# Performance work log

Hardware: AMD Instinct MI355X
Metric: run time of the kernel (lower is better)

Reference implementation:

```python
import jax, jax.numpy as jnp
import numpy as np

N, E, D, IN_DIM, NUM_CLASSES, G, L = 50000, 800000, 128, 128, 10, 64, 3
BN_EPS = 1e-5


def _bn(h, gamma, beta, mean, var):
    # inference-mode batchnorm with running stats
    return (h - mean) * jax.lax.rsqrt(var + BN_EPS) * gamma + beta


def setup_inputs() -> dict:
    key = jax.random.key(0)
    ks = jax.random.split(key, 24)
    s = 0.02
    x = jax.random.normal(ks[0], (N, IN_DIM), dtype=jnp.float32)
    c_2 = jax.random.randint(ks[1], (E,), 0, N)
    u_2 = jax.random.randint(ks[2], (E,), 0, N)
    batch = jnp.sort(jax.random.randint(ks[3], (N,), 0, G))
    inp = {
        "x": x, "c_2": c_2, "u_2": u_2, "batch": batch,
        "We": jax.random.normal(ks[4], (IN_DIM, D)) * s,
        "be": jnp.zeros((D,), jnp.float32),
        # per-layer GIN MLP: Linear(d,2d) -> BN(2d) -> ReLU -> Linear(2d,d)
        "W1": jax.random.normal(ks[5], (L, D, 2 * D)) * s,
        "b1": jnp.zeros((L, 2 * D), jnp.float32),
        "g1": jnp.ones((L, 2 * D), jnp.float32),
        "bt1": jnp.zeros((L, 2 * D), jnp.float32),
        "m1": jax.random.normal(ks[6], (L, 2 * D)) * 0.1,
        "v1": jax.random.uniform(ks[7], (L, 2 * D), minval=0.5, maxval=1.5),
        "W2": jax.random.normal(ks[8], (L, 2 * D, D)) * s,
        "b2": jnp.zeros((L, D), jnp.float32),
        # post-conv BatchNorm(d)
        "g2": jnp.ones((L, D), jnp.float32),
        "bt2": jnp.zeros((L, D), jnp.float32),
        "m2": jax.random.normal(ks[9], (L, D)) * 0.1,
        "v2": jax.random.uniform(ks[10], (L, D), minval=0.5, maxval=1.5),
        # readout: Linear(d,d) -> ReLU -> (dropout off) -> Linear(d,num_classes)
        "Wr1": jax.random.normal(ks[11], (D, D)) * s,
        "br1": jnp.zeros((D,), jnp.float32),
        "Wr2": jax.random.normal(ks[12], (D, NUM_CLASSES)) * s,
        "br2": jnp.zeros((NUM_CLASSES,), jnp.float32),
    }
    return inp


def reference(x, c_2, u_2, batch, We, be, W1, b1, g1, bt1, m1, v1,
              W2, b2, g2, bt2, m2, v2, Wr1, br1, Wr2, br2):
    h = x @ We + be  # [N, D]
    for l in range(L):
        # GINConv (eps=0): h_i <- MLP(h_i + sum_{j->i} h_j)
        agg = jax.ops.segment_sum(h[c_2], u_2, num_segments=N)  # [N, D]
        z = h + agg
        z = jax.nn.relu(_bn(z @ W1[l] + b1[l], g1[l], bt1[l], m1[l], v1[l]))
        z = z @ W2[l] + b2[l]
        h = jax.nn.relu(_bn(z, g2[l], bt2[l], m2[l], v2[l]))
        # dropout: identity in eval mode
    pooled = jax.ops.segment_sum(h, batch, num_segments=G)  # [G, D]
    out = jax.nn.relu(pooled @ Wr1 + br1) @ Wr2 + br2  # [G, num_classes]
    return out
```

## Files before the change

kernel.cpp:

```cpp
#include <hip/hip_runtime.h>

#define BN_EPS 1e-5f

typedef __attribute__((ext_vector_type(8))) short bf16x8;
typedef __attribute__((ext_vector_type(4))) float f32x4;
typedef unsigned int uint32;

__device__ __forceinline__ unsigned short f2bf(float f) {
    unsigned u = __float_as_uint(f);
    u += 0x7FFFu + ((u >> 16) & 1u);
    return (unsigned short)(u >> 16);
}
__device__ __forceinline__ float bf2f(unsigned short u) {
    return __uint_as_float((unsigned)u << 16);
}
__device__ __forceinline__ float lo_bf(uint32 u) { return __uint_as_float(u << 16); }
__device__ __forceinline__ float hi_bf(uint32 u) { return __uint_as_float(u & 0xFFFF0000u); }
__device__ __forceinline__ uint32 pack_bf(float a0, float a1) {
    return ((uint32)f2bf(a1) << 16) | (uint32)f2bf(a0);
}

__global__ __launch_bounds__(256) void count_coarse_kernel(const int* __restrict__ u2,
                                                           int* __restrict__ coarse_cnt, int E) {
    __shared__ int lcnt[256];
    const int tid = threadIdx.x;
    lcnt[tid] = 0;
    __syncthreads();
    const int e0 = blockIdx.x * 4096;
#pragma unroll
    for (int k = 0; k < 16; ++k) {
        int e = e0 + k * 256 + tid;
        if (e < E) atomicAdd(&lcnt[u2[e] >> 8], 1);
    }
    __syncthreads();
    int c = lcnt[tid];
    if (c) atomicAdd(&coarse_cnt[tid], c);
}

__global__ __launch_bounds__(256) void bin_coarse_kernel(const int* __restrict__ u2,
                                                         const int* __restrict__ c2,
                                                         const int* __restrict__ coarse_cnt,
                                                         int* __restrict__ coarse_alloc,
                                                         int* __restrict__ buck, int E, int nc) {
    __shared__ int sbuf[256];
    __shared__ int lcnt[256];
    __shared__ int lbase[256];
    const int tid = threadIdx.x;
    int cv = (tid < nc) ? coarse_cnt[tid] : 0;
    sbuf[tid] = cv;
    __syncthreads();
    for (int off = 1; off < 256; off <<= 1) {
        int x = (tid >= off) ? sbuf[tid - off] : 0;
        __syncthreads();
        sbuf[tid] += x;
        __syncthreads();
    }
    const int cstart = sbuf[tid] - cv;
    lcnt[tid] = 0;
    __syncthreads();
    const int e0 = blockIdx.x * 4096;
    int ue[16];
#pragma unroll
    for (int k = 0; k < 16; ++k) {
        int e = e0 + k * 256 + tid;
        int u = (e < E) ? u2[e] : -1;
        ue[k] = u;
        if (u >= 0) atomicAdd(&lcnt[u >> 8], 1);
    }
    __syncthreads();
    int c0 = lcnt[tid];
    lbase[tid] = cstart + (c0 ? atomicAdd(&coarse_alloc[tid], c0) : 0);
    lcnt[tid] = 0;
    __syncthreads();
#pragma unroll
    for (int k = 0; k < 16; ++k) {
        int e = e0 + k * 256 + tid;
        if (e < E) {
            int u = ue[k];
            int cb = u >> 8;
            int pos = lbase[cb] + atomicAdd(&lcnt[cb], 1);
            buck[pos] = ((u & 255) << 16) | c2[e];
        }
    }
}

__global__ __launch_bounds__(256) void bin_node_kernel(const int* __restrict__ coarse_cnt,
                                                       const int* __restrict__ buck,
                                                       int* __restrict__ node_start,
                                                       int* __restrict__ csr_src, int N, int nc) {
    __shared__ int sbuf[256];
    __shared__ int lcnt[256];
    __shared__ int lcur[256];
    const int cb = blockIdx.x;
    const int tid = threadIdx.x;
    int cv = (tid < nc) ? coarse_cnt[tid] : 0;
    sbuf[tid] = cv;
    __syncthreads();
    for (int off = 1; off < 256; off <<= 1) {
        int x = (tid >= off) ? sbuf[tid - off] : 0;
        __syncthreads();
        sbuf[tid] += x;
        __syncthreads();
    }
    lcnt[tid] = 0;
    __syncthreads();
    const int s = (cb == 0) ? 0 : sbuf[cb - 1];
    const int t_end = sbuf[cb];
    for (int e = s + tid; e < t_end; e += 256)
        atomicAdd(&lcnt[buck[e] >> 16], 1);
    __syncthreads();
    int v = lcnt[tid];
    lcur[tid] = v;
    __syncthreads();
    for (int off = 1; off < 256; off <<= 1) {
        int x = (tid >= off) ? lcur[tid - off] : 0;
        __syncthreads();
        lcur[tid] += x;
        __syncthreads();
    }
    int excl = lcur[tid] - v;
    int gstart = s + excl;
    int idx = cb * 256 + tid;
    if (idx <= N) node_start[idx] = gstart;
    lcur[tid] = gstart;
    __syncthreads();
    for (int e = s + tid; e < t_end; e += 256) {
        int w = buck[e];
        int pos = atomicAdd(&lcur[w >> 16], 1);
        csr_src[pos] = w & 0xFFFF;
    }
}

__global__ __launch_bounds__(256) void aggregate_kernel(const unsigned short* __restrict__ h,
                                                        const int* __restrict__ row_start,
                                                        const int* __restrict__ csr_src,
                                                        unsigned short* __restrict__ h2, int N) {
    int node = blockIdx.x * 4 + (threadIdx.x >> 6);
    int lane = threadIdx.x & 63;
    if (node >= N) return;
    const int q = lane >> 4, sl = lane & 15;

    float a0 = 0.f, a1 = 0.f, a2 = 0.f, a3 = 0.f, a4 = 0.f, a5 = 0.f, a6 = 0.f, a7 = 0.f;
    if (q == 0) {
        uint4 v = ((const uint4*)(h + (size_t)node * 128))[sl];
        a0 = lo_bf(v.x); a1 = hi_bf(v.x); a2 = lo_bf(v.y); a3 = hi_bf(v.y);
        a4 = lo_bf(v.z); a5 = hi_bf(v.z); a6 = lo_bf(v.w); a7 = hi_bf(v.w);
    }

    const int rs = row_start[node], re = row_start[node + 1];
    int e = rs;
    for (; e + 16 <= re; e += 16) {
        int s0 = csr_src[e + q];
        int s1 = csr_src[e + 4 + q];
        int s2 = csr_src[e + 8 + q];
        int s3 = csr_src[e + 12 + q];
        uint4 v0 = ((const uint4*)(h + (size_t)s0 * 128))[sl];
        uint4 v1 = ((const uint4*)(h + (size_t)s1 * 128))[sl];
        uint4 v2 = ((const uint4*)(h + (size_t)s2 * 128))[sl];
        uint4 v3 = ((const uint4*)(h + (size_t)s3 * 128))[sl];
        a0 += (lo_bf(v0.x) + lo_bf(v1.x)) + (lo_bf(v2.x) + lo_bf(v3.x));
        a1 += (hi_bf(v0.x) + hi_bf(v1.x)) + (hi_bf(v2.x) + hi_bf(v3.x));
        a2 += (lo_bf(v0.y) + lo_bf(v1.y)) + (lo_bf(v2.y) + lo_bf(v3.y));
        a3 += (hi_bf(v0.y) + hi_bf(v1.y)) + (hi_bf(v2.y) + hi_bf(v3.y));
        a4 += (lo_bf(v0.z) + lo_bf(v1.z)) + (lo_bf(v2.z) + lo_bf(v3.z));
        a5 += (hi_bf(v0.z) + hi_bf(v1.z)) + (hi_bf(v2.z) + hi_bf(v3.z));
        a6 += (lo_bf(v0.w) + lo_bf(v1.w)) + (lo_bf(v2.w) + lo_bf(v3.w));
        a7 += (hi_bf(v0.w) + hi_bf(v1.w)) + (hi_bf(v2.w) + hi_bf(v3.w));
    }
    for (; e + 8 <= re; e += 8) {
        int s0 = csr_src[e + q];
        int s1 = csr_src[e + 4 + q];
        uint4 v = ((const uint4*)(h + (size_t)s0 * 128))[sl];
        uint4 w = ((const uint4*)(h + (size_t)s1 * 128))[sl];
        a0 += lo_bf(v.x) + lo_bf(w.x); a1 += hi_bf(v.x) + hi_bf(w.x);
        a2 += lo_bf(v.y) + lo_bf(w.y); a3 += hi_bf(v.y) + hi_bf(w.y);
        a4 += lo_bf(v.z) + lo_bf(w.z); a5 += hi_bf(v.z) + hi_bf(w.z);
        a6 += lo_bf(v.w) + lo_bf(w.w); a7 += hi_bf(v.w) + hi_bf(w.w);
    }
    for (; e + 4 <= re; e += 4) {
        int s0 = csr_src[e + q];
        uint4 v = ((const uint4*)(h + (size_t)s0 * 128))[sl];
        a0 += lo_bf(v.x); a1 += hi_bf(v.x); a2 += lo_bf(v.y); a3 += hi_bf(v.y);
        a4 += lo_bf(v.z); a5 += hi_bf(v.z); a6 += lo_bf(v.w); a7 += hi_bf(v.w);
    }
    if (q < re - e) {
        int s0 = csr_src[e + q];
        uint4 v = ((const uint4*)(h + (size_t)s0 * 128))[sl];
        a0 += lo_bf(v.x); a1 += hi_bf(v.x); a2 += lo_bf(v.y); a3 += hi_bf(v.y);
        a4 += lo_bf(v.z); a5 += hi_bf(v.z); a6 += lo_bf(v.w); a7 += hi_bf(v.w);
    }

    a0 += __shfl_xor(a0, 16, 64); a0 += __shfl_xor(a0, 32, 64);
    a1 += __shfl_xor(a1, 16, 64); a1 += __shfl_xor(a1, 32, 64);
    a2 += __shfl_xor(a2, 16, 64); a2 += __shfl_xor(a2, 32, 64);
    a3 += __shfl_xor(a3, 16, 64); a3 += __shfl_xor(a3, 32, 64);
    a4 += __shfl_xor(a4, 16, 64); a4 += __shfl_xor(a4, 32, 64);
    a5 += __shfl_xor(a5, 16, 64); a5 += __shfl_xor(a5, 32, 64);
    a6 += __shfl_xor(a6, 16, 64); a6 += __shfl_xor(a6, 32, 64);
    a7 += __shfl_xor(a7, 16, 64); a7 += __shfl_xor(a7, 32, 64);

    if (q == 0) {
        uint4 o;
        o.x = pack_bf(a0, a1); o.y = pack_bf(a2, a3);
        o.z = pack_bf(a4, a5); o.w = pack_bf(a6, a7);
        ((uint4*)(h2 + (size_t)node * 128))[sl] = o;
    }
}

__global__ void prep_kernel(const float* __restrict__ We, const float* __restrict__ W1,
                            const float* __restrict__ W2,
                            unsigned short* __restrict__ Wte,
                            unsigned short* __restrict__ Wt1,
                            unsigned short* __restrict__ Wt2,
                            const float* __restrict__ be,
                            const float* __restrict__ b1, const float* __restrict__ g1,
                            const float* __restrict__ bt1, const float* __restrict__ m1,
                            const float* __restrict__ v1,
                            const float* __restrict__ b2, const float* __restrict__ g2,
                            const float* __restrict__ bt2, const float* __restrict__ m2,
                            const float* __restrict__ v2,
                            float* __restrict__ sce, float* __restrict__ she,
                            float* __restrict__ sc1, float* __restrict__ sh1,
                            float* __restrict__ sc2, float* __restrict__ sh2, int L) {
    int y = blockIdx.y;
    int t = threadIdx.x;
    if (blockIdx.x == 0) {
        if (y == 0) {
            if (t < 128) { sce[t] = 1.f; she[t] = be[t]; }
        } else if (y <= L) {
            int o = (y - 1) * 256 + t;
            float s = g1[o] * rsqrtf(v1[o] + BN_EPS);
            sc1[o] = s;
            sh1[o] = (b1[o] - m1[o]) * s + bt1[o];
        } else {
            if (t < 128) {
                int o = (y - L - 1) * 128 + t;
                float s = g2[o] * rsqrtf(v2[o] + BN_EPS);
                sc2[o] = s;
                sh2[o] = (b2[o] - m2[o]) * s + bt2[o];
            }
        }
    }
    const float* src;
    unsigned short* dst;
    int K;
    if (y == 0)      { src = We; dst = Wte; K = 128; }
    else if (y <= L) { int l = y - 1;     src = W1 + (size_t)l * 128 * 256; dst = Wt1 + (size_t)l * 128 * 256; K = 128; }
    else             { int l = y - L - 1; src = W2 + (size_t)l * 256 * 128; dst = Wt2 + (size_t)l * 256 * 128; K = 256; }
    int idx = blockIdx.x * 256 + t;
    int OUT = 32768 / K;
    if (y == 0) { if (idx >= 128 * 128) return; OUT = 128; }
    int c = idx / K, k = idx % K;
    unsigned byte = ((unsigned)(idx * 2)) ^ (((unsigned)c & 7u) << 4);
    *(unsigned short*)((char*)dst + byte) = f2bf(src[(size_t)k * OUT + c]);
}

template <int K, int OUT, bool RELU, bool A_F32>
__global__ __launch_bounds__(256) void mfma_gemm_kernel(
    const void* __restrict__ Ap, const unsigned short* __restrict__ Wt,
    const float* __restrict__ scale, const float* __restrict__ shift,
    unsigned short* __restrict__ Cout, int nrows)
{
    constexpr int NT = OUT / 16;
    constexpr int KS = K / 32;
    constexpr int CH = OUT * K / 8;
    __shared__ unsigned short WtLds[OUT * K];

    const int tid = threadIdx.x;
    const int wv = tid >> 6, lane = tid & 63;
    {
#pragma unroll
        for (int i = 0; i < CH / 256; ++i) {
            unsigned chunk = (unsigned)(i * 256 + wv * 64);
            const char* gsrc = (const char*)Wt + (size_t)(chunk + lane) * 16u;
            char* ldst = (char*)WtLds + (size_t)chunk * 16u;
            __builtin_amdgcn_global_load_lds(
                (const __attribute__((address_space(1))) void*)gsrc,
                (__attribute__((address_space(3))) void*)ldst,
                16, 0, 0);
        }
    }

    const int l15 = lane & 15, lhi = lane >> 4;
    const int rbase = blockIdx.x * 128 + wv * 32;
    const int r0 = rbase + l15;
    const int r1 = rbase + 16 + l15;
    const int rr0 = min(r0, nrows - 1);
    const int rr1 = min(r1, nrows - 1);

    bf16x8 bfrag[2][KS];
    if constexpr (A_F32) {
        const float* a0 = (const float*)Ap + (size_t)rr0 * K + lhi * 8;
        const float* a1 = (const float*)Ap + (size_t)rr1 * K + lhi * 8;
#pragma unroll
        for (int ks = 0; ks < KS; ++ks) {
            float4 u0 = *(const float4*)(a0 + ks * 32);
            float4 u1 = *(const float4*)(a0 + ks * 32 + 4);
            float4 w0 = *(const float4*)(a1 + ks * 32);
            float4 w1 = *(const float4*)(a1 + ks * 32 + 4);
            bf16x8 f, g;
            f[0] = (short)f2bf(u0.x); f[1] = (short)f2bf(u0.y);
            f[2] = (short)f2bf(u0.z); f[3] = (short)f2bf(u0.w);
            f[4] = (short)f2bf(u1.x); f[5] = (short)f2bf(u1.y);
            f[6] = (short)f2bf(u1.z); f[7] = (short)f2bf(u1.w);
            g[0] = (short)f2bf(w0.x); g[1] = (short)f2bf(w0.y);
            g[2] = (short)f2bf(w0.z); g[3] = (short)f2bf(w0.w);
            g[4] = (short)f2bf(w1.x); g[5] = (short)f2bf(w1.y);
            g[6] = (short)f2bf(w1.z); g[7] = (short)f2bf(w1.w);
            bfrag[0][ks] = f;
            bfrag[1][ks] = g;
        }
    } else {
        const unsigned short* a0 = (const unsigned short*)Ap + (size_t)rr0 * K + lhi * 8;
        const unsigned short* a1 = (const unsigned short*)Ap + (size_t)rr1 * K + lhi * 8;
#pragma unroll
        for (int ks = 0; ks < KS; ++ks) {
            bfrag[0][ks] = *(const bf16x8*)(a0 + ks * 32);
            bfrag[1][ks] = *(const bf16x8*)(a1 + ks * 32);
        }
    }

    __syncthreads();

    f32x4 acc[2][NT];
#pragma unroll
    for (int g = 0; g < 2; ++g)
#pragma unroll
        for (int nt = 0; nt < NT; ++nt) acc[g][nt] = (f32x4){0.f, 0.f, 0.f, 0.f};

#pragma unroll
    for (int ks = 0; ks < KS; ++ks) {
#pragma unroll
        for (int nt = 0; nt < NT; ++nt) {
            int row = nt * 16 + l15;
            unsigned off = ((unsigned)((row * K + ks * 32 + lhi * 8) * 2)) ^ (((unsigned)(l15 & 7u)) << 4);
            bf16x8 wfrag = *(const bf16x8*)((const char*)WtLds + off);
            acc[0][nt] = __builtin_amdgcn_mfma_f32_16x16x32_bf16(wfrag, bfrag[0][ks], acc[0][nt], 0, 0, 0);
            acc[1][nt] = __builtin_amdgcn_mfma_f32_16x16x32_bf16(wfrag, bfrag[1][ks], acc[1][nt], 0, 0, 0);
        }
    }

    const float4* sc4 = (const float4*)scale;
    const float4* sh4 = (const float4*)shift;
#pragma unroll
    for (int g = 0; g < 2; ++g) {
        const int r = (g == 0) ? r0 : r1;
        if (r >= nrows) continue;
#pragma unroll
        for (int nt = 0; nt < NT; ++nt) {
            float4 sc = sc4[nt * 4 + lhi];
            float4 sh = sh4[nt * 4 + lhi];
            float y0 = acc[g][nt][0] * sc.x + sh.x;
            float y1 = acc[g][nt][1] * sc.y + sh.y;
            float y2 = acc[g][nt][2] * sc.z + sh.z;
            float y3 = acc[g][nt][3] * sc.w + sh.w;
            if (RELU) {
                y0 = fmaxf(y0, 0.f); y1 = fmaxf(y1, 0.f);
                y2 = fmaxf(y2, 0.f); y3 = fmaxf(y3, 0.f);
            }
            size_t o = (size_t)r * OUT + nt * 16 + lhi * 4;
            ushort4 p = make_ushort4(f2bf(y0), f2bf(y1), f2bf(y2), f2bf(y3));
            *(ushort4*)(Cout + o) = p;
        }
    }
}

__global__ __launch_bounds__(128) void pool_kernel(const unsigned short* __restrict__ h,
                                                   const int* __restrict__ batch,
                                                   float* __restrict__ pooled, int N, int chunk) {
    int d = threadIdx.x;
    int start = blockIdx.x * chunk;
    if (start >= N) return;
    int end = min(start + chunk, N);
    float acc = 0.f;
    int g = batch[start];
    for (int r = start; r < end; ++r) {
        int bg = batch[r];
        if (bg != g) {
            atomicAdd(&pooled[g * 128 + d], acc);
            acc = 0.f;
            g = bg;
        }
        acc += bf2f(h[(size_t)r * 128 + d]);
    }
    atomicAdd(&pooled[g * 128 + d], acc);
}

__global__ __launch_bounds__(128) void readout_kernel(const float* __restrict__ pooled,
                                                      const float* __restrict__ Wr1,
                                                      const float* __restrict__ br1,
                                                      const float* __restrict__ Wr2,
                                                      const float* __restrict__ br2,
                                                      float* __restrict__ out) {
    __shared__ float prow[128];
    __shared__ float t[128];
    int g = blockIdx.x, j = threadIdx.x;
    prow[j] = pooled[g * 128 + j];
    __syncthreads();
    float acc = 0.f;
    for (int k = 0; k < 128; ++k) acc += prow[k] * Wr1[k * 128 + j];
    t[j] = fmaxf(acc + br1[j], 0.f);
    __syncthreads();
    if (j < 10) {
        float a2 = 0.f;
        for (int k = 0; k < 128; ++k) a2 += t[k] * Wr2[k * 10 + j];
        out[g * 10 + j] = a2 + br2[j];
    }
}

extern "C" void kernel_launch(void* const* d_in, const int* in_sizes, int n_in,
                              void* d_out, int out_size, void* d_ws, size_t ws_size,
                              hipStream_t stream) {
    const float* x   = (const float*)d_in[0];
    const int* c2    = (const int*)d_in[1];
    const int* u2    = (const int*)d_in[2];
    const int* batch = (const int*)d_in[3];
    const float* We  = (const float*)d_in[4];
    const float* be  = (const float*)d_in[5];
    const float* W1  = (const float*)d_in[6];
    const float* b1  = (const float*)d_in[7];
    const float* g1  = (const float*)d_in[8];
    const float* bt1 = (const float*)d_in[9];
    const float* m1  = (const float*)d_in[10];
    const float* v1  = (const float*)d_in[11];
    const float* W2  = (const float*)d_in[12];
    const float* b2  = (const float*)d_in[13];
    const float* g2  = (const float*)d_in[14];
    const float* bt2 = (const float*)d_in[15];
    const float* m2  = (const float*)d_in[16];
    const float* v2  = (const float*)d_in[17];
    const float* Wr1 = (const float*)d_in[18];
    const float* br1 = (const float*)d_in[19];
    const float* Wr2 = (const float*)d_in[20];
    const float* br2 = (const float*)d_in[21];

    const int N = in_sizes[3];
    const int E = in_sizes[1];
    const int L = in_sizes[7] / 256;
    const int G = out_size / 10;

    const int NC = (N + 255) / 256;

    char* ws = (char*)d_ws;
    size_t off = 0;
    auto alloc = [&](size_t bytes) { char* p = ws + off; off += (bytes + 255) & ~(size_t)255; return p; };
    unsigned short* hb   = (unsigned short*)alloc((size_t)N * 128 * 2);
    unsigned short* h2b  = (unsigned short*)alloc((size_t)N * 128 * 2);
    unsigned short* zb   = (unsigned short*)alloc((size_t)N * 256 * 2);
    unsigned short* Wte  = (unsigned short*)alloc(128 * 128 * 2);
    unsigned short* Wt1  = (unsigned short*)alloc((size_t)L * 256 * 128 * 2);
    unsigned short* Wt2  = (unsigned short*)alloc((size_t)L * 128 * 256 * 2);
    float* sce = (float*)alloc(128 * 4);
    float* she = (float*)alloc(128 * 4);
    float* sc1 = (float*)alloc((size_t)L * 256 * 4);
    float* sh1 = (float*)alloc((size_t)L * 256 * 4);
    float* sc2 = (float*)alloc((size_t)L * 128 * 4);
    float* sh2 = (float*)alloc((size_t)L * 128 * 4);
    float* pooled = (float*)alloc((size_t)G * 128 * 4);
    int* coarse_cnt   = (int*)alloc(512 * 4);
    int* coarse_alloc = coarse_cnt + 256;
    int* node_start   = (int*)alloc((size_t)(N + 1) * 4);
    int* buck         = (int*)alloc((size_t)E * 4);
    int* csr_src      = (int*)alloc((size_t)E * 4);

    const int ebins = (E + 4095) / 4096;

    hipMemsetAsync(coarse_cnt, 0, 512 * 4, stream);
    hipMemsetAsync(pooled, 0, (size_t)G * 128 * 4, stream);
    count_coarse_kernel<<<ebins, 256, 0, stream>>>(u2, coarse_cnt, E);
    bin_coarse_kernel<<<ebins, 256, 0, stream>>>(u2, c2, coarse_cnt, coarse_alloc, buck, E, NC);
    bin_node_kernel<<<NC, 256, 0, stream>>>(coarse_cnt, buck, node_start, csr_src, N, NC);

    prep_kernel<<<dim3((256 * 128 + 255) / 256, 1 + 2 * L), 256, 0, stream>>>(
        We, W1, W2, Wte, Wt1, Wt2,
        be, b1, g1, bt1, m1, v1, b2, g2, bt2, m2, v2,
        sce, she, sc1, sh1, sc2, sh2, L);

    const int gemm_blocks = (N + 127) / 128;

    mfma_gemm_kernel<128, 128, false, true><<<gemm_blocks, 256, 0, stream>>>(
        x, Wte, sce, she, hb, N);

    for (int l = 0; l < L; ++l) {
        aggregate_kernel<<<(N + 3) / 4, 256, 0, stream>>>(hb, node_start, csr_src, h2b, N);
        mfma_gemm_kernel<128, 256, true, false><<<gemm_blocks, 256, 0, stream>>>(
            h2b, Wt1 + (size_t)l * 128 * 256, sc1 + l * 256, sh1 + l * 256, zb, N);
        mfma_gemm_kernel<256, 128, true, false><<<gemm_blocks, 256, 0, stream>>>(
            zb, Wt2 + (size_t)l * 256 * 128, sc2 + l * 128, sh2 + l * 128, hb, N);
    }

    const int pool_blocks = 2048;
    const int chunk = (N + pool_blocks - 1) / pool_blocks;
    pool_kernel<<<pool_blocks, 128, 0, stream>>>(hb, batch, pooled, N, chunk);
    readout_kernel<<<G, 128, 0, stream>>>(pooled, Wr1, br1, Wr2, br2, (float*)d_out);
}
```

Before: 277.1 us.

## Split GEMM output columns across waves, shrink row tile to 64

Changes the MFMA GEMM work split: each block now handles 64 rows instead of 128, and each of the four waves computes a quarter of the output columns for all 64 rows instead of all columns for 32 rows. Each LDS weight fragment is reused across four row groups rather than two, and the grid doubles, which helps fill the GPU. The trade-offs are that the full weight matrix is staged into LDS twice as many times in total, each wave loads all 64 A rows (duplicate A reads across waves), and register pressure rises from the larger fragment arrays.

```diff
diff --git a/kernel.cpp b/kernel.cpp
--- a/kernel.cpp
+++ b/kernel.cpp
@@ -261,8 +261,9 @@
     const float* __restrict__ scale, const float* __restrict__ shift,
     unsigned short* __restrict__ Cout, int nrows)
 {
-    constexpr int NT = OUT / 16;
+    constexpr int NT = OUT / 64;
     constexpr int KS = K / 32;
+    constexpr int RG = 4;
     constexpr int CH = OUT * K / 8;
     __shared__ unsigned short WtLds[OUT * K];
 
@@ -282,83 +283,75 @@
     }
 
     const int l15 = lane & 15, lhi = lane >> 4;
-    const int rbase = blockIdx.x * 128 + wv * 32;
-    const int r0 = rbase + l15;
-    const int r1 = rbase + 16 + l15;
-    const int rr0 = min(r0, nrows - 1);
-    const int rr1 = min(r1, nrows - 1);
-
-    bf16x8 bfrag[2][KS];
-    if constexpr (A_F32) {
-        const float* a0 = (const float*)Ap + (size_t)rr0 * K + lhi * 8;
-        const float* a1 = (const float*)Ap + (size_t)rr1 * K + lhi * 8;
-#pragma unroll
-        for (int ks = 0; ks < KS; ++ks) {
-            float4 u0 = *(const float4*)(a0 + ks * 32);
-            float4 u1 = *(const float4*)(a0 + ks * 32 + 4);
-            float4 w0 = *(const float4*)(a1 + ks * 32);
-            float4 w1 = *(const float4*)(a1 + ks * 32 + 4);
-            bf16x8 f, g;
-            f[0] = (short)f2bf(u0.x); f[1] = (short)f2bf(u0.y);
-            f[2] = (short)f2bf(u0.z); f[3] = (short)f2bf(u0.w);
-            f[4] = (short)f2bf(u1.x); f[5] = (short)f2bf(u1.y);
-            f[6] = (short)f2bf(u1.z); f[7] = (short)f2bf(u1.w);
-            g[0] = (short)f2bf(w0.x); g[1] = (short)f2bf(w0.y);
-            g[2] = (short)f2bf(w0.z); g[3] = (short)f2bf(w0.w);
-            g[4] = (short)f2bf(w1.x); g[5] = (short)f2bf(w1.y);
-            g[6] = (short)f2bf(w1.z); g[7] = (short)f2bf(w1.w);
-            bfrag[0][ks] = f;
-            bfrag[1][ks] = g;
-        }
-    } else {
-        const unsigned short* a0 = (const unsigned short*)Ap + (size_t)rr0 * K + lhi * 8;
-        const unsigned short* a1 = (const unsigned short*)Ap + (size_t)rr1 * K + lhi * 8;
-#pragma unroll
-        for (int ks = 0; ks < KS; ++ks) {
-            bfrag[0][ks] = *(const bf16x8*)(a0 + ks * 32);
-            bfrag[1][ks] = *(const bf16x8*)(a1 + ks * 32);
-        }
-    }
-
-    __syncthreads();
-
-    f32x4 acc[2][NT];
-#pragma unroll
-    for (int g = 0; g < 2; ++g)
-#pragma unroll
-        for (int nt = 0; nt < NT; ++nt) acc[g][nt] = (f32x4){0.f, 0.f, 0.f, 0.f};
+    const int wc0 = wv * (OUT / 4);
+    const int rbase = blockIdx.x * 64;
+
+    bf16x8 bfrag[RG][KS];
+#pragma unroll
+    for (int rg = 0; rg < RG; ++rg) {
+        const int rr = min(rbase + rg * 16 + l15, nrows - 1);
+        if constexpr (A_F32) {
+            const float* arow = (const float*)Ap + (size_t)rr * K + lhi * 8;
+#pragma unroll
+            for (int ks = 0; ks < KS; ++ks) {
+                float4 u0 = *(const float4*)(arow + ks * 32);
+                float4 u1 = *(const float4*)(arow + ks * 32 + 4);
+                bf16x8 f;
+                f[0] = (short)f2bf(u0.x); f[1] = (short)f2bf(u0.y);
+                f[2] = (short)f2bf(u0.z); f[3] = (short)f2bf(u0.w);
+                f[4] = (short)f2bf(u1.x); f[5] = (short)f2bf(u1.y);
+                f[6] = (short)f2bf(u1.z); f[7] = (short)f2bf(u1.w);
+                bfrag[rg][ks] = f;
+            }
+        } else {
+            const unsigned short* arow = (const unsigned short*)Ap + (size_t)rr * K + lhi * 8;
+#pragma unroll
+            for (int ks = 0; ks < KS; ++ks)
+                bfrag[rg][ks] = *(const bf16x8*)(arow + ks * 32);
+        }
+    }
+
+    __syncthreads();
+
+    f32x4 acc[RG][NT];
+#pragma unroll
+    for (int rg = 0; rg < RG; ++rg)
+#pragma unroll
+        for (int nt = 0; nt < NT; ++nt) acc[rg][nt] = (f32x4){0.f, 0.f, 0.f, 0.f};
 
 #pragma unroll
     for (int ks = 0; ks < KS; ++ks) {
 #pragma unroll
         for (int nt = 0; nt < NT; ++nt) {
-            int row = nt * 16 + l15;
+            int row = wc0 + nt * 16 + l15;
             unsigned off = ((unsigned)((row * K + ks * 32 + lhi * 8) * 2)) ^ (((unsigned)(l15 & 7u)) << 4);
             bf16x8 wfrag = *(const bf16x8*)((const char*)WtLds + off);
-            acc[0][nt] = __builtin_amdgcn_mfma_f32_16x16x32_bf16(wfrag, bfrag[0][ks], acc[0][nt], 0, 0, 0);
-            acc[1][nt] = __builtin_amdgcn_mfma_f32_16x16x32_bf16(wfrag, bfrag[1][ks], acc[1][nt], 0, 0, 0);
+#pragma unroll
+            for (int rg = 0; rg < RG; ++rg)
+                acc[rg][nt] = __builtin_amdgcn_mfma_f32_16x16x32_bf16(wfrag, bfrag[rg][ks], acc[rg][nt], 0, 0, 0);
         }
     }
 
     const float4* sc4 = (const float4*)scale;
     const float4* sh4 = (const float4*)shift;
 #pragma unroll
-    for (int g = 0; g < 2; ++g) {
-        const int r = (g == 0) ? r0 : r1;
+    for (int rg = 0; rg < RG; ++rg) {
+        const int r = rbase + rg * 16 + l15;
         if (r >= nrows) continue;
 #pragma unroll
         for (int nt = 0; nt < NT; ++nt) {
-            float4 sc = sc4[nt * 4 + lhi];
-            float4 sh = sh4[nt * 4 + lhi];
-            float y0 = acc[g][nt][0] * sc.x + sh.x;
-            float y1 = acc[g][nt][1] * sc.y + sh.y;
-            float y2 = acc[g][nt][2] * sc.z + sh.z;
-            float y3 = acc[g][nt][3] * sc.w + sh.w;
+            const int cq = wc0 / 4 + nt * 4 + lhi;
+            float4 sc = sc4[cq];
+            float4 sh = sh4[cq];
+            float y0 = acc[rg][nt][0] * sc.x + sh.x;
+            float y1 = acc[rg][nt][1] * sc.y + sh.y;
+            float y2 = acc[rg][nt][2] * sc.z + sh.z;
+            float y3 = acc[rg][nt][3] * sc.w + sh.w;
             if (RELU) {
                 y0 = fmaxf(y0, 0.f); y1 = fmaxf(y1, 0.f);
                 y2 = fmaxf(y2, 0.f); y3 = fmaxf(y3, 0.f);
             }
-            size_t o = (size_t)r * OUT + nt * 16 + lhi * 4;
+            size_t o = (size_t)r * OUT + wc0 + nt * 16 + lhi * 4;
             ushort4 p = make_ushort4(f2bf(y0), f2bf(y1), f2bf(y2), f2bf(y3));
             *(ushort4*)(Cout + o) = p;
         }
@@ -476,7 +469,7 @@
         be, b1, g1, bt1, m1, v1, b2, g2, bt2, m2, v2,
         sce, she, sc1, sh1, sc2, sh2, L);
 
-    const int gemm_blocks = (N + 127) / 128;
+    const int gemm_blocks = (N + 63) / 64;
 
     mfma_gemm_kernel<128, 128, false, true><<<gemm_blocks, 256, 0, stream>>>(
         x, Wte, sce, she, hb, N);
```

Result: slower. 320.2 us (+15.5%).

## Merge independent setup kernels into two combined launches

Applied to the files above, without the earlier changes.

Fuses the coarse edge-count kernel with the weight/BN preparation kernel into one launch, and the coarse binning kernel with the input embedding GEMM into a second launch. Blocks pick their role by block index. This cuts two kernel launches and lets independent setup work overlap on the GPU. The cost is heavier register and LDS use in the combined kernels, since the binning blocks now carry the GEMM's 32 KB LDS allocation.

```diff
diff --git a/kernel.cpp b/kernel.cpp
--- a/kernel.cpp
+++ b/kernel.cpp
@@ -20,66 +20,211 @@
     return ((uint32)f2bf(a1) << 16) | (uint32)f2bf(a0);
 }
 
-__global__ __launch_bounds__(256) void count_coarse_kernel(const int* __restrict__ u2,
-                                                           int* __restrict__ coarse_cnt, int E) {
+__global__ __launch_bounds__(256) void setup_a_kernel(
+    const int* __restrict__ u2, int* __restrict__ coarse_cnt, int E, int nca,
+    const float* __restrict__ We, const float* __restrict__ W1, const float* __restrict__ W2,
+    unsigned short* __restrict__ Wte, unsigned short* __restrict__ Wt1,
+    unsigned short* __restrict__ Wt2,
+    const float* __restrict__ be,
+    const float* __restrict__ b1, const float* __restrict__ g1, const float* __restrict__ bt1,
+    const float* __restrict__ m1, const float* __restrict__ v1,
+    const float* __restrict__ b2, const float* __restrict__ g2, const float* __restrict__ bt2,
+    const float* __restrict__ m2, const float* __restrict__ v2,
+    float* __restrict__ sce, float* __restrict__ she,
+    float* __restrict__ sc1, float* __restrict__ sh1,
+    float* __restrict__ sc2, float* __restrict__ sh2, int L)
+{
     __shared__ int lcnt[256];
-    const int tid = threadIdx.x;
-    lcnt[tid] = 0;
-    __syncthreads();
-    const int e0 = blockIdx.x * 4096;
-#pragma unroll
-    for (int k = 0; k < 16; ++k) {
-        int e = e0 + k * 256 + tid;
-        if (e < E) atomicAdd(&lcnt[u2[e] >> 8], 1);
-    }
-    __syncthreads();
-    int c = lcnt[tid];
-    if (c) atomicAdd(&coarse_cnt[tid], c);
-}
-
-__global__ __launch_bounds__(256) void bin_coarse_kernel(const int* __restrict__ u2,
-                                                         const int* __restrict__ c2,
-                                                         const int* __restrict__ coarse_cnt,
-                                                         int* __restrict__ coarse_alloc,
-                                                         int* __restrict__ buck, int E, int nc) {
+    const int t = threadIdx.x;
+    if ((int)blockIdx.x < nca) {
+        lcnt[t] = 0;
+        __syncthreads();
+        const int e0 = blockIdx.x * 4096;
+#pragma unroll
+        for (int k = 0; k < 16; ++k) {
+            int e = e0 + k * 256 + t;
+            if (e < E) atomicAdd(&lcnt[u2[e] >> 8], 1);
+        }
+        __syncthreads();
+        int c = lcnt[t];
+        if (c) atomicAdd(&coarse_cnt[t], c);
+        return;
+    }
+    const int pb = blockIdx.x - nca;
+    const int y = pb >> 7;
+    const int bx = pb & 127;
+    if (bx == 0) {
+        if (y == 0) {
+            if (t < 128) { sce[t] = 1.f; she[t] = be[t]; }
+        } else if (y <= L) {
+            int o = (y - 1) * 256 + t;
+            float s = g1[o] * rsqrtf(v1[o] + BN_EPS);
+            sc1[o] = s;
+            sh1[o] = (b1[o] - m1[o]) * s + bt1[o];
+        } else {
+            if (t < 128) {
+                int o = (y - L - 1) * 128 + t;
+                float s = g2[o] * rsqrtf(v2[o] + BN_EPS);
+                sc2[o] = s;
+                sh2[o] = (b2[o] - m2[o]) * s + bt2[o];
+            }
+        }
+    }
+    const float* src;
+    unsigned short* dst;
+    int K;
+    if (y == 0)      { src = We; dst = Wte; K = 128; }
+    else if (y <= L) { int l = y - 1;     src = W1 + (size_t)l * 128 * 256; dst = Wt1 + (size_t)l * 128 * 256; K = 128; }
+    else             { int l = y - L - 1; src = W2 + (size_t)l * 256 * 128; dst = Wt2 + (size_t)l * 256 * 128; K = 256; }
+    int idx = bx * 256 + t;
+    int OUT = 32768 / K;
+    if (y == 0) { if (idx >= 128 * 128) return; OUT = 128; }
+    int c = idx / K, k = idx % K;
+    unsigned byte = ((unsigned)(idx * 2)) ^ (((unsigned)c & 7u) << 4);
+    *(unsigned short*)((char*)dst + byte) = f2bf(src[(size_t)k * OUT + c]);
+}
+
+__global__ __launch_bounds__(256) void setup_b_kernel(
+    const int* __restrict__ u2, const int* __restrict__ c2,
+    const int* __restrict__ coarse_cnt, int* __restrict__ coarse_alloc,
+    int* __restrict__ buck, int E, int nc, int nca,
+    const float* __restrict__ x, const unsigned short* __restrict__ Wte,
+    const float* __restrict__ sce, const float* __restrict__ she,
+    unsigned short* __restrict__ hb, int nrows)
+{
+    __shared__ unsigned short WtLds[128 * 128];
     __shared__ int sbuf[256];
     __shared__ int lcnt[256];
     __shared__ int lbase[256];
     const int tid = threadIdx.x;
-    int cv = (tid < nc) ? coarse_cnt[tid] : 0;
-    sbuf[tid] = cv;
-    __syncthreads();
-    for (int off = 1; off < 256; off <<= 1) {
-        int x = (tid >= off) ? sbuf[tid - off] : 0;
-        __syncthreads();
-        sbuf[tid] += x;
-        __syncthreads();
-    }
-    const int cstart = sbuf[tid] - cv;
-    lcnt[tid] = 0;
-    __syncthreads();
-    const int e0 = blockIdx.x * 4096;
-    int ue[16];
-#pragma unroll
-    for (int k = 0; k < 16; ++k) {
-        int e = e0 + k * 256 + tid;
-        int u = (e < E) ? u2[e] : -1;
-        ue[k] = u;
-        if (u >= 0) atomicAdd(&lcnt[u >> 8], 1);
-    }
-    __syncthreads();
-    int c0 = lcnt[tid];
-    lbase[tid] = cstart + (c0 ? atomicAdd(&coarse_alloc[tid], c0) : 0);
-    lcnt[tid] = 0;
-    __syncthreads();
-#pragma unroll
-    for (int k = 0; k < 16; ++k) {
-        int e = e0 + k * 256 + tid;
-        if (e < E) {
-            int u = ue[k];
-            int cb = u >> 8;
-            int pos = lbase[cb] + atomicAdd(&lcnt[cb], 1);
-            buck[pos] = ((u & 255) << 16) | c2[e];
+
+    if ((int)blockIdx.x < nca) {
+        int cv = (tid < nc) ? coarse_cnt[tid] : 0;
+        sbuf[tid] = cv;
+        __syncthreads();
+        for (int off = 1; off < 256; off <<= 1) {
+            int xv = (tid >= off) ? sbuf[tid - off] : 0;
+            __syncthreads();
+            sbuf[tid] += xv;
+            __syncthreads();
+        }
+        const int cstart = sbuf[tid] - cv;
+        lcnt[tid] = 0;
+        __syncthreads();
+        const int e0 = blockIdx.x * 4096;
+        int ue[16];
+#pragma unroll
+        for (int k = 0; k < 16; ++k) {
+            int e = e0 + k * 256 + tid;
+            int u = (e < E) ? u2[e] : -1;
+            ue[k] = u;
+            if (u >= 0) atomicAdd(&lcnt[u >> 8], 1);
+        }
+        __syncthreads();
+        int c0 = lcnt[tid];
+        lbase[tid] = cstart + (c0 ? atomicAdd(&coarse_alloc[tid], c0) : 0);
+        lcnt[tid] = 0;
+        __syncthreads();
+#pragma unroll
+        for (int k = 0; k < 16; ++k) {
+            int e = e0 + k * 256 + tid;
+            if (e < E) {
+                int u = ue[k];
+                int cb = u >> 8;
+                int pos = lbase[cb] + atomicAdd(&lcnt[cb], 1);
+                buck[pos] = ((u & 255) << 16) | c2[e];
+            }
+        }
+        return;
+    }
+
+    constexpr int K = 128, OUT = 128;
+    constexpr int NT = OUT / 16;
+    constexpr int KS = K / 32;
+    constexpr int CH = OUT * K / 8;
+    const int bid = blockIdx.x - nca;
+    const int wv = tid >> 6, lane = tid & 63;
+    {
+#pragma unroll
+        for (int i = 0; i < CH / 256; ++i) {
+            unsigned chunk = (unsigned)(i * 256 + wv * 64);
+            const char* gsrc = (const char*)Wte + (size_t)(chunk + lane) * 16u;
+            char* ldst = (char*)WtLds + (size_t)chunk * 16u;
+            __builtin_amdgcn_global_load_lds(
+                (const __attribute__((address_space(1))) void*)gsrc,
+                (__attribute__((address_space(3))) void*)ldst,
+                16, 0, 0);
+        }
+    }
+
+    const int l15 = lane & 15, lhi = lane >> 4;
+    const int rbase = bid * 128 + wv * 32;
+    const int r0 = rbase + l15;
+    const int r1 = rbase + 16 + l15;
+    const int rr0 = min(r0, nrows - 1);
+    const int rr1 = min(r1, nrows - 1);
+
+    bf16x8 bfrag[2][KS];
+    {
+        const float* a0 = x + (size_t)rr0 * K + lhi * 8;
+        const float* a1 = x + (size_t)rr1 * K + lhi * 8;
+#pragma unroll
+        for (int ks = 0; ks < KS; ++ks) {
+            float4 u0 = *(const float4*)(a0 + ks * 32);
+            float4 u1 = *(const float4*)(a0 + ks * 32 + 4);
+            float4 w0 = *(const float4*)(a1 + ks * 32);
+            float4 w1 = *(const float4*)(a1 + ks * 32 + 4);
+            bf16x8 f, g;
+            f[0] = (short)f2bf(u0.x); f[1] = (short)f2bf(u0.y);
+            f[2] = (short)f2bf(u0.z); f[3] = (short)f2bf(u0.w);
+            f[4] = (short)f2bf(u1.x); f[5] = (short)f2bf(u1.y);
+            f[6] = (short)f2bf(u1.z); f[7] = (short)f2bf(u1.w);
+            g[0] = (short)f2bf(w0.x); g[1] = (short)f2bf(w0.y);
+            g[2] = (short)f2bf(w0.z); g[3] = (short)f2bf(w0.w);
+            g[4] = (short)f2bf(w1.x); g[5] = (short)f2bf(w1.y);
+            g[6] = (short)f2bf(w1.z); g[7] = (short)f2bf(w1.w);
+            bfrag[0][ks] = f;
+            bfrag[1][ks] = g;
+        }
+    }
+
+    __syncthreads();
+
+    f32x4 acc[2][NT];
+#pragma unroll
+    for (int g = 0; g < 2; ++g)
+#pragma unroll
+        for (int nt = 0; nt < NT; ++nt) acc[g][nt] = (f32x4){0.f, 0.f, 0.f, 0.f};
+
+#pragma unroll
+    for (int ks = 0; ks < KS; ++ks) {
+#pragma unroll
+        for (int nt = 0; nt < NT; ++nt) {
+            int row = nt * 16 + l15;
+            unsigned off = ((unsigned)((row * K + ks * 32 + lhi * 8) * 2)) ^ (((unsigned)(l15 & 7u)) << 4);
+            bf16x8 wfrag = *(const bf16x8*)((const char*)WtLds + off);
+            acc[0][nt] = __builtin_amdgcn_mfma_f32_16x16x32_bf16(wfrag, bfrag[0][ks], acc[0][nt], 0, 0, 0);
+            acc[1][nt] = __builtin_amdgcn_mfma_f32_16x16x32_bf16(wfrag, bfrag[1][ks], acc[1][nt], 0, 0, 0);
+        }
+    }
+
+    const float4* sc4 = (const float4*)sce;
+    const float4* sh4 = (const float4*)she;
+#pragma unroll
+    for (int g = 0; g < 2; ++g) {
+        const int r = (g == 0) ? r0 : r1;
+        if (r >= nrows) continue;
+#pragma unroll
+        for (int nt = 0; nt < NT; ++nt) {
+            float4 sc = sc4[nt * 4 + lhi];
+            float4 sh = sh4[nt * 4 + lhi];
+            float y0 = acc[g][nt][0] * sc.x + sh.x;
+            float y1 = acc[g][nt][1] * sc.y + sh.y;
+            float y2 = acc[g][nt][2] * sc.z + sh.z;
+            float y3 = acc[g][nt][3] * sc.w + sh.w;
+            size_t o = (size_t)r * OUT + nt * 16 + lhi * 4;
+            ushort4 p = make_ushort4(f2bf(y0), f2bf(y1), f2bf(y2), f2bf(y3));
+            *(ushort4*)(hb + o) = p;
         }
     }
 }
@@ -207,57 +352,9 @@
     }
 }
 
-__global__ void prep_kernel(const float* __restrict__ We, const float* __restrict__ W1,
-                            const float* __restrict__ W2,
-                            unsigned short* __restrict__ Wte,
-                            unsigned short* __restrict__ Wt1,
-                            unsigned short* __restrict__ Wt2,
-                            const float* __restrict__ be,
-                            const float* __restrict__ b1, const float* __restrict__ g1,
-                            const float* __restrict__ bt1, const float* __restrict__ m1,
-                            const float* __restrict__ v1,
-                            const float* __restrict__ b2, const float* __restrict__ g2,
-                            const float* __restrict__ bt2, const float* __restrict__ m2,
-                            const float* __restrict__ v2,
-                            float* __restrict__ sce, float* __restrict__ she,
-                            float* __restrict__ sc1, float* __restrict__ sh1,
-                            float* __restrict__ sc2, float* __restrict__ sh2, int L) {
-    int y = blockIdx.y;
-    int t = threadIdx.x;
-    if (blockIdx.x == 0) {
-        if (y == 0) {
-            if (t < 128) { sce[t] = 1.f; she[t] = be[t]; }
-        } else if (y <= L) {
-            int o = (y - 1) * 256 + t;
-            float s = g1[o] * rsqrtf(v1[o] + BN_EPS);
-            sc1[o] = s;
-            sh1[o] = (b1[o] - m1[o]) * s + bt1[o];
-        } else {
-            if (t < 128) {
-                int o = (y - L - 1) * 128 + t;
-                float s = g2[o] * rsqrtf(v2[o] + BN_EPS);
-                sc2[o] = s;
-                sh2[o] = (b2[o] - m2[o]) * s + bt2[o];
-            }
-        }
-    }
-    const float* src;
-    unsigned short* dst;
-    int K;
-    if (y == 0)      { src = We; dst = Wte; K = 128; }
-    else if (y <= L) { int l = y - 1;     src = W1 + (size_t)l * 128 * 256; dst = Wt1 + (size_t)l * 128 * 256; K = 128; }
-    else             { int l = y - L - 1; src = W2 + (size_t)l * 256 * 128; dst = Wt2 + (size_t)l * 256 * 128; K = 256; }
-    int idx = blockIdx.x * 256 + t;
-    int OUT = 32768 / K;
-    if (y == 0) { if (idx >= 128 * 128) return; OUT = 128; }
-    int c = idx / K, k = idx % K;
-    unsigned byte = ((unsigned)(idx * 2)) ^ (((unsigned)c & 7u) << 4);
-    *(unsigned short*)((char*)dst + byte) = f2bf(src[(size_t)k * OUT + c]);
-}
-
-template <int K, int OUT, bool RELU, bool A_F32>
+template <int K, int OUT, bool RELU>
 __global__ __launch_bounds__(256) void mfma_gemm_kernel(
-    const void* __restrict__ Ap, const unsigned short* __restrict__ Wt,
+    const unsigned short* __restrict__ Ap, const unsigned short* __restrict__ Wt,
     const float* __restrict__ scale, const float* __restrict__ shift,
     unsigned short* __restrict__ Cout, int nrows)
 {
@@ -289,30 +386,9 @@
     const int rr1 = min(r1, nrows - 1);
 
     bf16x8 bfrag[2][KS];
-    if constexpr (A_F32) {
-        const float* a0 = (const float*)Ap + (size_t)rr0 * K + lhi * 8;
-        const float* a1 = (const float*)Ap + (size_t)rr1 * K + lhi * 8;
-#pragma unroll
-        for (int ks = 0; ks < KS; ++ks) {
-            float4 u0 = *(const float4*)(a0 + ks * 32);
-            float4 u1 = *(const float4*)(a0 + ks * 32 + 4);
-            float4 w0 = *(const float4*)(a1 + ks * 32);
-            float4 w1 = *(const float4*)(a1 + ks * 32 + 4);
-            bf16x8 f, g;
-            f[0] = (short)f2bf(u0.x); f[1] = (short)f2bf(u0.y);
-            f[2] = (short)f2bf(u0.z); f[3] = (short)f2bf(u0.w);
-            f[4] = (short)f2bf(u1.x); f[5] = (short)f2bf(u1.y);
-            f[6] = (short)f2bf(u1.z); f[7] = (short)f2bf(u1.w);
-            g[0] = (short)f2bf(w0.x); g[1] = (short)f2bf(w0.y);
-            g[2] = (short)f2bf(w0.z); g[3] = (short)f2bf(w0.w);
-            g[4] = (short)f2bf(w1.x); g[5] = (short)f2bf(w1.y);
-            g[6] = (short)f2bf(w1.z); g[7] = (short)f2bf(w1.w);
-            bfrag[0][ks] = f;
-            bfrag[1][ks] = g;
-        }
-    } else {
-        const unsigned short* a0 = (const unsigned short*)Ap + (size_t)rr0 * K + lhi * 8;
-        const unsigned short* a1 = (const unsigned short*)Ap + (size_t)rr1 * K + lhi * 8;
+    {
+        const unsigned short* a0 = Ap + (size_t)rr0 * K + lhi * 8;
+        const unsigned short* a1 = Ap + (size_t)rr1 * K + lhi * 8;
 #pragma unroll
         for (int ks = 0; ks < KS; ++ks) {
             bfrag[0][ks] = *(const bf16x8*)(a0 + ks * 32);
@@ -464,28 +540,29 @@
     int* csr_src      = (int*)alloc((size_t)E * 4);
 
     const int ebins = (E + 4095) / 4096;
+    const int gemm_blocks = (N + 127) / 128;
+    const int prep_blocks = 128 * (1 + 2 * L);
 
     hipMemsetAsync(coarse_cnt, 0, 512 * 4, stream);
     hipMemsetAsync(pooled, 0, (size_t)G * 128 * 4, stream);
-    count_coarse_kernel<<<ebins, 256, 0, stream>>>(u2, coarse_cnt, E);
-    bin_coarse_kernel<<<ebins, 256, 0, stream>>>(u2, c2, coarse_cnt, coarse_alloc, buck, E, NC);
-    bin_node_kernel<<<NC, 256, 0, stream>>>(coarse_cnt, buck, node_start, csr_src, N, NC);
-
-    prep_kernel<<<dim3((256 * 128 + 255) / 256, 1 + 2 * L), 256, 0, stream>>>(
+
+    setup_a_kernel<<<ebins + prep_blocks, 256, 0, stream>>>(
+        u2, coarse_cnt, E, ebins,
         We, W1, W2, Wte, Wt1, Wt2,
         be, b1, g1, bt1, m1, v1, b2, g2, bt2, m2, v2,
         sce, she, sc1, sh1, sc2, sh2, L);
 
-    const int gemm_blocks = (N + 127) / 128;
-
-    mfma_gemm_kernel<128, 128, false, true><<<gemm_blocks, 256, 0, stream>>>(
+    setup_b_kernel<<<ebins + gemm_blocks, 256, 0, stream>>>(
+        u2, c2, coarse_cnt, coarse_alloc, buck, E, NC, ebins,
         x, Wte, sce, she, hb, N);
+
+    bin_node_kernel<<<NC, 256, 0, stream>>>(coarse_cnt, buck, node_start, csr_src, N, NC);
 
     for (int l = 0; l < L; ++l) {
         aggregate_kernel<<<(N + 3) / 4, 256, 0, stream>>>(hb, node_start, csr_src, h2b, N);
-        mfma_gemm_kernel<128, 256, true, false><<<gemm_blocks, 256, 0, stream>>>(
+        mfma_gemm_kernel<128, 256, true><<<gemm_blocks, 256, 0, stream>>>(
             h2b, Wt1 + (size_t)l * 128 * 256, sc1 + l * 256, sh1 + l * 256, zb, N);
-        mfma_gemm_kernel<256, 128, true, false><<<gemm_blocks, 256, 0, stream>>>(
+        mfma_gemm_kernel<256, 128, true><<<gemm_blocks, 256, 0, stream>>>(
             zb, Wt2 + (size_t)l * 256 * 128, sc2 + l * 128, sh2 + l * 128, hb, N);
     }
 
```

After: 266.9 us. 1.04x faster.
